# Optimization experiments

Measured on AMD Instinct MI355X. Metric: run time of the kernel, lower is better.

The kernel has to match this reference:

```python
import jax, jax.numpy as jnp
import numpy as np

B, N, C = 2, 2048, 1024
H = 16
HD = C // H  # 64


def setup_inputs() -> dict:
    key = jax.random.key(0)
    k1, k2, k3 = jax.random.split(key, 3)
    x = jax.random.normal(k1, (B, N, C), dtype=jnp.float32)
    w_qkv = jax.random.normal(k2, (C, 3 * C), dtype=jnp.float32) * (C ** -0.5)
    b_qkv = jnp.zeros((3 * C,), dtype=jnp.float32)
    w_out = jax.random.normal(k3, (C, C), dtype=jnp.float32) * (C ** -0.5)
    b_out = jnp.zeros((C,), dtype=jnp.float32)
    return {"x": x, "w_qkv": w_qkv, "b_qkv": b_qkv, "w_out": w_out, "b_out": b_out}


def reference(x, w_qkv, b_qkv, w_out, b_out):
    scale = HD ** -0.5
    # QKV projection: (B,N,3C) -> (B,N,3,H,HD) -> (B,3,H,N,HD)
    qkv = (jnp.einsum('bnc,cd->bnd', x, w_qkv) + b_qkv)
    qkv = qkv.reshape(B, N, 3, H, HD).transpose(0, 2, 3, 1, 4)
    q, k, v = qkv[:, 0], qkv[:, 1], qkv[:, 2]  # each (B,H,N,HD)
    # scaled dot-product attention with full NxN matrix (as in source)
    attn = jnp.einsum('bhnd,bhmd->bhnm', q, k) * scale
    attn = jax.nn.softmax(attn, axis=-1)
    out = jnp.einsum('bhnm,bhmd->bhnd', attn, v)  # (B,H,N,HD)
    out = out.transpose(0, 2, 1, 3).reshape(B, N, C)
    out = jnp.einsum('bnc,cd->bnd', out, w_out) + b_out
    return out
```

## Files before the change

kernel.cpp:

```cpp
#include <hip/hip_runtime.h>
#include <stdint.h>

using uint = unsigned int;
using ushort = unsigned short;

constexpr int Bb = 2;
constexpr int Ns = 2048;
constexpr int Cd = 1024;
constexpr int Hh = 16;
constexpr int HD = 64;
constexpr int BHND = Bb * Hh * Ns * HD;

constexpr float QSCL = 0.18033688f;

typedef __attribute__((ext_vector_type(8))) short short8;
typedef __attribute__((ext_vector_type(4))) float floatx4;

__device__ inline ushort f2bf(float f) {
  uint u = __float_as_uint(f);
  return (ushort)((u + 0x7fffu + ((u >> 16) & 1u)) >> 16);
}
__device__ inline ushort f2bfr(float f) {
  return (ushort)((__float_as_uint(f) + 0x8000u) >> 16);
}
__device__ inline uint cvt_pk_bf16(float lo, float hi) {
  uint r;
  asm("v_cvt_pk_bf16_f32 %0, %1, %2" : "=v"(r) : "v"(lo), "v"(hi));
  return r;
}
__device__ inline void gld_lds16(const ushort* g, ushort* l) {
  __builtin_amdgcn_global_load_lds(
      (const __attribute__((address_space(1))) uint*)g,
      (__attribute__((address_space(3))) uint*)l, 16, 0, 0);
}

__global__ __launch_bounds__(256) void prep(
    const float* __restrict__ x, ushort* __restrict__ xbf,
    const float* __restrict__ w_qkv, ushort* __restrict__ wqkvT,
    const float* __restrict__ w_out, ushort* __restrict__ woutT) {
  __shared__ alignas(16) ushort tile[32][33];
  const int bid = blockIdx.x;
  const int tid = threadIdx.x;
  if (bid < 4096) {
    const int i = bid * 256 + tid;
    const float4 v = ((const float4*)x)[i];
    ushort4 o;
    o.x = f2bf(v.x); o.y = f2bf(v.y); o.z = f2bf(v.z); o.w = f2bf(v.w);
    ((ushort4*)xbf)[i] = o;
    return;
  }
  const float* in;
  ushort* outp;
  int Cc, idx;
  if (bid < 7168) { idx = bid - 4096; in = w_qkv; outp = wqkvT; Cc = 3072; }
  else            { idx = bid - 7168; in = w_out; outp = woutT; Cc = 1024; }
  const int R = 1024;
  const int nbx = Cc >> 5;
  const int bx = idx % nbx, by = idx / nbx;
  const int c0 = bx * 32, r0 = by * 32;
  const int tx = tid & 31, ty = tid >> 5;
#pragma unroll
  for (int i = 0; i < 4; ++i)
    tile[ty + 8 * i][tx] = f2bf(in[(size_t)(r0 + ty + 8 * i) * Cc + c0 + tx]);
  __syncthreads();
#pragma unroll
  for (int i = 0; i < 4; ++i)
    outp[(size_t)(c0 + ty + 8 * i) * R + r0 + tx] = tile[tx][ty + 8 * i];
}

__global__ __launch_bounds__(256, 3) void gemm_qkv(
    const ushort* __restrict__ A, const ushort* __restrict__ Bt,
    const float* __restrict__ bias, ushort* __restrict__ outp,
    int M, int K, int Nn) {
  __shared__ alignas(16) ushort As[3][128 * 32];
  __shared__ alignas(16) ushort Bs[3][128 * 32];
  const int tid = threadIdx.x;
  const int wave = tid >> 6, lane = tid & 63;
  const int quad = lane >> 4, l16 = lane & 15;
  const int wr = wave >> 1, wc = wave & 1;
  const int m0 = blockIdx.x * 128, n0 = blockIdx.y * 128;

  const int lrow = lane >> 2;
  const int lgr = lane & 3;
  const ushort* pa = A + (size_t)(m0 + wave * 32 + lrow) * K + lgr * 8;
  const ushort* pb = Bt + (size_t)(n0 + wave * 32 + lrow) * K + lgr * 8;
  const int lofs = wave * 32 * 32;

  floatx4 acc[4][4];
#pragma unroll
  for (int i = 0; i < 4; ++i)
#pragma unroll
    for (int j = 0; j < 4; ++j) {
      acc[i][j][0] = 0.f; acc[i][j][1] = 0.f; acc[i][j][2] = 0.f; acc[i][j][3] = 0.f;
    }

  const int nkt = K >> 5;
  gld_lds16(pa, &As[0][lofs]);
  gld_lds16(pa + (size_t)16 * K, &As[0][lofs + 512]);
  gld_lds16(pb, &Bs[0][lofs]);
  gld_lds16(pb + (size_t)16 * K, &Bs[0][lofs + 512]);
  gld_lds16(pa + 32, &As[1][lofs]);
  gld_lds16(pa + 32 + (size_t)16 * K, &As[1][lofs + 512]);
  gld_lds16(pb + 32, &Bs[1][lofs]);
  gld_lds16(pb + 32 + (size_t)16 * K, &Bs[1][lofs + 512]);

  int cur = 0;
  auto compute_tile = [&](int cb) {
    short8 af[4], bfv[4];
    const ushort* Ab = &As[cb][0];
    const ushort* Bb2 = &Bs[cb][0];
#pragma unroll
    for (int mt = 0; mt < 4; ++mt)
      af[mt] = *(const short8*)&Ab[(wr * 64 + mt * 16 + l16) * 32 + quad * 8];
#pragma unroll
    for (int nt = 0; nt < 4; ++nt)
      bfv[nt] = *(const short8*)&Bb2[(wc * 64 + nt * 16 + l16) * 32 + quad * 8];
#pragma unroll
    for (int mt = 0; mt < 4; ++mt)
#pragma unroll
      for (int nt = 0; nt < 4; ++nt)
        acc[mt][nt] = __builtin_amdgcn_mfma_f32_16x16x32_bf16(af[mt], bfv[nt],
                                                              acc[mt][nt], 0, 0, 0);
  };

  for (int kt = 0; kt < nkt - 1; ++kt) {
    asm volatile("s_waitcnt vmcnt(4)" ::: "memory");
    __builtin_amdgcn_s_barrier();
    __builtin_amdgcn_sched_barrier(0);
    compute_tile(cur);
    __builtin_amdgcn_s_barrier();
    if (kt + 2 < nkt) {
      const ushort* qa = pa + (size_t)(kt + 2) * 32;
      const ushort* qb = pb + (size_t)(kt + 2) * 32;
      int nb = cur + 2; if (nb >= 3) nb -= 3;
      gld_lds16(qa, &As[nb][lofs]);
      gld_lds16(qa + (size_t)16 * K, &As[nb][lofs + 512]);
      gld_lds16(qb, &Bs[nb][lofs]);
      gld_lds16(qb + (size_t)16 * K, &Bs[nb][lofs + 512]);
    }
    ++cur; if (cur == 3) cur = 0;
  }
  asm volatile("s_waitcnt vmcnt(0)" ::: "memory");
  __builtin_amdgcn_s_barrier();
  __builtin_amdgcn_sched_barrier(0);
  compute_tile(cur);

  ushort* qp = outp;
  ushort* kp = qp + BHND;
  ushort* vp = qp + 2 * BHND;
#pragma unroll
  for (int nt = 0; nt < 4; ++nt) {
    const int gn = n0 + wc * 64 + nt * 16 + l16;
    const float bv = bias[gn];
    const int which = gn >> 10, cc = gn & 1023;
    const int h = cc >> 6, d = cc & 63;
    const float sc = (which == 0) ? QSCL : 1.0f;
#pragma unroll
    for (int mt = 0; mt < 4; ++mt) {
#pragma unroll
      for (int r = 0; r < 4; ++r) {
        const int gm = m0 + wr * 64 + mt * 16 + quad * 4 + r;
        const int b = gm >> 11, n = gm & 2047;
        const ushort o = f2bfr((acc[mt][nt][r] + bv) * sc);
        const int bh = b * Hh + h;
        if (which == 0)
          qp[((size_t)bh * Ns + n) * HD + d] = o;
        else if (which == 1)
          kp[((size_t)bh * Ns + n) * HD + d] = o;
        else
          vp[((size_t)bh * HD + d) * Ns + n] = o;
      }
    }
  }
}

__global__ __launch_bounds__(256) void gemm_out(
    const ushort* __restrict__ A, const ushort* __restrict__ Bt,
    const float* __restrict__ bias, float* __restrict__ fout,
    int M, int K, int Nn) {
  constexpr int LDT = 40;
  __shared__ alignas(16) ushort As[128 * LDT];
  __shared__ alignas(16) ushort Bs[128 * LDT];
  const int tid = threadIdx.x;
  const int wave = tid >> 6, lane = tid & 63;
  const int quad = lane >> 4, l16 = lane & 15;
  const int wr = wave >> 1, wc = wave & 1;
  const int m0 = blockIdx.x * 128, n0 = blockIdx.y * 128;

  const int srow0 = tid >> 2;
  const int skc = (tid & 3) * 8;

  const ushort* pa = A + (size_t)(m0 + srow0) * K + skc;
  const ushort* pb = Bt + (size_t)(n0 + srow0) * K + skc;

  floatx4 acc[4][4];
#pragma unroll
  for (int i = 0; i < 4; ++i)
#pragma unroll
    for (int j = 0; j < 4; ++j) {
      acc[i][j][0] = 0.f; acc[i][j][1] = 0.f; acc[i][j][2] = 0.f; acc[i][j][3] = 0.f;
    }

  uint4 ra0 = *(const uint4*)(pa);
  uint4 ra1 = *(const uint4*)(pa + (size_t)64 * K);
  uint4 rb0 = *(const uint4*)(pb);
  uint4 rb1 = *(const uint4*)(pb + (size_t)64 * K);

  const int nkt = K >> 5;
  for (int kt = 0; kt < nkt; ++kt) {
    __syncthreads();
    *(uint4*)&As[srow0 * LDT + skc] = ra0;
    *(uint4*)&As[(srow0 + 64) * LDT + skc] = ra1;
    *(uint4*)&Bs[srow0 * LDT + skc] = rb0;
    *(uint4*)&Bs[(srow0 + 64) * LDT + skc] = rb1;
    __syncthreads();
    if (kt + 1 < nkt) {
      const ushort* qa = pa + (size_t)(kt + 1) * 32;
      const ushort* qb = pb + (size_t)(kt + 1) * 32;
      ra0 = *(const uint4*)(qa);
      ra1 = *(const uint4*)(qa + (size_t)64 * K);
      rb0 = *(const uint4*)(qb);
      rb1 = *(const uint4*)(qb + (size_t)64 * K);
    }
    short8 af[4], bfv[4];
#pragma unroll
    for (int mt = 0; mt < 4; ++mt)
      af[mt] = *(const short8*)&As[(wr * 64 + mt * 16 + l16) * LDT + quad * 8];
#pragma unroll
    for (int nt = 0; nt < 4; ++nt)
      bfv[nt] = *(const short8*)&Bs[(wc * 64 + nt * 16 + l16) * LDT + quad * 8];
#pragma unroll
    for (int mt = 0; mt < 4; ++mt)
#pragma unroll
      for (int nt = 0; nt < 4; ++nt)
        acc[mt][nt] = __builtin_amdgcn_mfma_f32_16x16x32_bf16(af[mt], bfv[nt],
                                                              acc[mt][nt], 0, 0, 0);
  }

#pragma unroll
  for (int nt = 0; nt < 4; ++nt) {
    const int gn = n0 + wc * 64 + nt * 16 + l16;
    const float bv = bias[gn];
#pragma unroll
    for (int mt = 0; mt < 4; ++mt)
#pragma unroll
      for (int r = 0; r < 4; ++r) {
        const int gm = m0 + wr * 64 + mt * 16 + quad * 4 + r;
        fout[(size_t)gm * Nn + gn] = acc[mt][nt][r] + bv;
      }
  }
}

__global__ __launch_bounds__(256, 2) void attn(
    const ushort* __restrict__ q, const ushort* __restrict__ k,
    const ushort* __restrict__ vT, ushort* __restrict__ aout) {
  constexpr int LDK = 72;
  __shared__ alignas(16) ushort Ks[2][64 * LDK];
  __shared__ alignas(16) ushort Vs[2][64 * LDK];
  const int tid = threadIdx.x;
  const int wave = tid >> 6, lane = tid & 63;
  const int quad = lane >> 4, l16 = lane & 15;

  const int orig = blockIdx.x + (blockIdx.y << 4);
  const int swz = (orig & 7) * 64 + (orig >> 3);
  const int bh = swz >> 4;
  const int qw = (swz & 15) * 128 + wave * 32;

  const ushort* kb = k + (size_t)bh * Ns * HD;
  const ushort* vb = vT + (size_t)bh * HD * Ns;

  short8 aq[2][2];
#pragma unroll
  for (int nqi = 0; nqi < 2; ++nqi) {
    const ushort* qp = q + ((size_t)bh * Ns + qw + nqi * 16 + l16) * HD + quad * 8;
    aq[nqi][0] = *(const short8*)(qp);
    aq[nqi][1] = *(const short8*)(qp + 32);
  }

  floatx4 accO[4][2];
#pragma unroll
  for (int mt = 0; mt < 4; ++mt)
#pragma unroll
    for (int nqi = 0; nqi < 2; ++nqi) {
      accO[mt][nqi][0] = 0.f; accO[mt][nqi][1] = 0.f;
      accO[mt][nqi][2] = 0.f; accO[mt][nqi][3] = 0.f;
    }
  float lst[2] = {0.f, 0.f};
  const floatx4 fz = {0.f, 0.f, 0.f, 0.f};

  const int srow = tid >> 2;
  const int g0 = (tid & 3) * 2;
  const int cbA = (g0 >> 2) * 8 + ((g0 >> 1) & 1);
  const int g1 = g0 + 1;
  const int cbB = (g1 >> 2) * 8 + 4 + ((g1 >> 1) & 1);

  const ushort* kgp = kb + (size_t)srow * HD + g0 * 8;
  const ushort* vgp = vb + (size_t)srow * Ns + g0 * 8;
  const int kofs = srow * LDK + g0 * 8;
  const int vofsA = srow * LDK + cbA * 4;
  const int vofsB = srow * LDK + cbB * 4;

  uint4 kg0 = *(const uint4*)(kgp);
  uint4 kg1 = *(const uint4*)(kgp + 8);
  uint4 vg0 = *(const uint4*)(vgp);
  uint4 vg1 = *(const uint4*)(vgp + 8);
  const ushort* kpre = kgp + 64 * HD;
  const ushort* vpre = vgp + 64;

  *(uint4*)&Ks[0][kofs] = kg0;
  *(uint4*)&Ks[0][kofs + 8] = kg1;
  *(uint2*)&Vs[0][vofsA] = make_uint2(vg0.x, vg0.y);
  *(uint2*)&Vs[0][vofsA + 8] = make_uint2(vg0.z, vg0.w);
  *(uint2*)&Vs[0][vofsB] = make_uint2(vg1.x, vg1.y);
  *(uint2*)&Vs[0][vofsB + 8] = make_uint2(vg1.z, vg1.w);
  __syncthreads();

  for (int kv0 = 0; kv0 < Ns; kv0 += 128) {
#pragma unroll
    for (int half = 0; half < 2; ++half) {
      const bool more = kv0 + 64 * (half + 1) < Ns;

      short8 ak[4][2], av[4][2];
#pragma unroll
      for (int t4 = 0; t4 < 4; ++t4) {
        const int ro = (t4 * 16 + l16) * LDK + quad * 8;
        ak[t4][0] = *(const short8*)&Ks[half][ro];
        ak[t4][1] = *(const short8*)&Ks[half][ro + 32];
        av[t4][0] = *(const short8*)&Vs[half][ro];
        av[t4][1] = *(const short8*)&Vs[half][ro + 32];
      }
      if (more) {
        kg0 = *(const uint4*)(kpre);
        kg1 = *(const uint4*)(kpre + 8);
        vg0 = *(const uint4*)(vpre);
        vg1 = *(const uint4*)(vpre + 8);
        kpre += 64 * HD;
        vpre += 64;
      }

#pragma unroll
      for (int nqi = 0; nqi < 2; ++nqi) {
        floatx4 sacc[4];
        __builtin_amdgcn_s_setprio(1);
#pragma unroll
        for (int kvt = 0; kvt < 4; ++kvt)
          sacc[kvt] = __builtin_amdgcn_mfma_f32_16x16x32_bf16(
              ak[kvt][0], aq[nqi][0], fz, 0, 0, 0);
#pragma unroll
        for (int kvt = 0; kvt < 4; ++kvt)
          sacc[kvt] = __builtin_amdgcn_mfma_f32_16x16x32_bf16(
              ak[kvt][1], aq[nqi][1], sacc[kvt], 0, 0, 0);
        __builtin_amdgcn_s_setprio(0);

        uint pk[4][2];
        float ls = 0.f;
#pragma unroll
        for (int kvt = 0; kvt < 4; ++kvt) {
          const float p0 = __builtin_amdgcn_exp2f(sacc[kvt][0]);
          const float p1 = __builtin_amdgcn_exp2f(sacc[kvt][1]);
          const float p2 = __builtin_amdgcn_exp2f(sacc[kvt][2]);
          const float p3 = __builtin_amdgcn_exp2f(sacc[kvt][3]);
          ls += (p0 + p1) + (p2 + p3);
          pk[kvt][0] = cvt_pk_bf16(p0, p1);
          pk[kvt][1] = cvt_pk_bf16(p2, p3);
        }
        lst[nqi] += ls;

        __builtin_amdgcn_s_setprio(1);
#pragma unroll
        for (int ks = 0; ks < 2; ++ks) {
          union { uint u[4]; short8 s; } pf;
          pf.u[0] = pk[2 * ks][0]; pf.u[1] = pk[2 * ks][1];
          pf.u[2] = pk[2 * ks + 1][0]; pf.u[3] = pk[2 * ks + 1][1];
#pragma unroll
          for (int mt = 0; mt < 4; ++mt)
            accO[mt][nqi] = __builtin_amdgcn_mfma_f32_16x16x32_bf16(
                av[mt][ks], pf.s, accO[mt][nqi], 0, 0, 0);
        }
        __builtin_amdgcn_s_setprio(0);
      }

      if (more) {
        *(uint4*)&Ks[half ^ 1][kofs] = kg0;
        *(uint4*)&Ks[half ^ 1][kofs + 8] = kg1;
        *(uint2*)&Vs[half ^ 1][vofsA] = make_uint2(vg0.x, vg0.y);
        *(uint2*)&Vs[half ^ 1][vofsA + 8] = make_uint2(vg0.z, vg0.w);
        *(uint2*)&Vs[half ^ 1][vofsB] = make_uint2(vg1.x, vg1.y);
        *(uint2*)&Vs[half ^ 1][vofsB + 8] = make_uint2(vg1.z, vg1.w);
      }
      __syncthreads();
    }
  }

  const int b = bh >> 4, h = bh & 15;
#pragma unroll
  for (int nqi = 0; nqi < 2; ++nqi) {
    float l = lst[nqi];
    l += __shfl_xor(l, 16, 64);
    l += __shfl_xor(l, 32, 64);
    const float inv = 1.f / l;
    const int n = qw + nqi * 16 + l16;
#pragma unroll
    for (int mt = 0; mt < 4; ++mt) {
      ushort4 o;
      o.x = f2bfr(accO[mt][nqi][0] * inv);
      o.y = f2bfr(accO[mt][nqi][1] * inv);
      o.z = f2bfr(accO[mt][nqi][2] * inv);
      o.w = f2bfr(accO[mt][nqi][3] * inv);
      *(ushort4*)&aout[((size_t)(b * Ns + n)) * Cd + h * HD + mt * 16 + quad * 4] = o;
    }
  }
}

extern "C" void kernel_launch(void* const* d_in, const int* in_sizes, int n_in,
                              void* d_out, int out_size, void* d_ws, size_t ws_size,
                              hipStream_t stream) {
  (void)in_sizes; (void)n_in; (void)out_size; (void)ws_size;
  const float* x = (const float*)d_in[0];
  const float* w_qkv = (const float*)d_in[1];
  const float* b_qkv = (const float*)d_in[2];
  const float* w_out = (const float*)d_in[3];
  const float* b_out = (const float*)d_in[4];

  ushort* xbf = (ushort*)d_ws;
  ushort* wqkvT = xbf + (size_t)BHND;
  ushort* woutT = wqkvT + 3072 * 1024;
  ushort* qkvbuf = woutT + 1024 * 1024;
  ushort* aout = qkvbuf + 3 * (size_t)BHND;

  prep<<<dim3(8192), 256, 0, stream>>>(x, xbf, w_qkv, wqkvT, w_out, woutT);

  gemm_qkv<<<dim3(32, 24), 256, 0, stream>>>(xbf, wqkvT, b_qkv, qkvbuf,
                                             4096, 1024, 3072);
  attn<<<dim3(16, 32), 256, 0, stream>>>(qkvbuf, qkvbuf + BHND,
                                         qkvbuf + 2 * (size_t)BHND, aout);
  gemm_out<<<dim3(32, 8), 256, 0, stream>>>(aout, woutT, b_out, (float*)d_out,
                                            4096, 1024, 1024);
}
```

Measured before the change: 182.4 us.

## Triple-buffer output GEMM with direct global-to-LDS async loads

Restructures the output projection GEMM so each wave loads its 32-row slice of the A and B tiles straight into LDS through gld_lds16, rotating across three LDS buffers. The next tiles are prefetched two k-steps ahead, and vmcnt-based waits replace the register-staged double sync. The aim is to overlap global loads with MFMA compute, drop the VGPR staging copy, and allow two blocks per CU through launch bounds. The padded LDS stride is removed, which may bring bank conflicts back on the fragment reads.

```diff
diff --git a/kernel.cpp b/kernel.cpp
--- a/kernel.cpp
+++ b/kernel.cpp
@@ -174,24 +174,23 @@
   }
 }
 
-__global__ __launch_bounds__(256) void gemm_out(
+__global__ __launch_bounds__(256, 2) void gemm_out(
     const ushort* __restrict__ A, const ushort* __restrict__ Bt,
     const float* __restrict__ bias, float* __restrict__ fout,
     int M, int K, int Nn) {
-  constexpr int LDT = 40;
-  __shared__ alignas(16) ushort As[128 * LDT];
-  __shared__ alignas(16) ushort Bs[128 * LDT];
+  __shared__ alignas(16) ushort As[3][128 * 32];
+  __shared__ alignas(16) ushort Bs[3][128 * 32];
   const int tid = threadIdx.x;
   const int wave = tid >> 6, lane = tid & 63;
   const int quad = lane >> 4, l16 = lane & 15;
   const int wr = wave >> 1, wc = wave & 1;
   const int m0 = blockIdx.x * 128, n0 = blockIdx.y * 128;
 
-  const int srow0 = tid >> 2;
-  const int skc = (tid & 3) * 8;
-
-  const ushort* pa = A + (size_t)(m0 + srow0) * K + skc;
-  const ushort* pb = Bt + (size_t)(n0 + srow0) * K + skc;
+  const int lrow = lane >> 2;
+  const int lgr = lane & 3;
+  const ushort* pa = A + (size_t)(m0 + wave * 32 + lrow) * K + lgr * 8;
+  const ushort* pb = Bt + (size_t)(n0 + wave * 32 + lrow) * K + lgr * 8;
+  const int lofs = wave * 32 * 32;
 
   floatx4 acc[4][4];
 #pragma unroll
@@ -201,41 +200,56 @@
       acc[i][j][0] = 0.f; acc[i][j][1] = 0.f; acc[i][j][2] = 0.f; acc[i][j][3] = 0.f;
     }
 
-  uint4 ra0 = *(const uint4*)(pa);
-  uint4 ra1 = *(const uint4*)(pa + (size_t)64 * K);
-  uint4 rb0 = *(const uint4*)(pb);
-  uint4 rb1 = *(const uint4*)(pb + (size_t)64 * K);
-
   const int nkt = K >> 5;
-  for (int kt = 0; kt < nkt; ++kt) {
-    __syncthreads();
-    *(uint4*)&As[srow0 * LDT + skc] = ra0;
-    *(uint4*)&As[(srow0 + 64) * LDT + skc] = ra1;
-    *(uint4*)&Bs[srow0 * LDT + skc] = rb0;
-    *(uint4*)&Bs[(srow0 + 64) * LDT + skc] = rb1;
-    __syncthreads();
-    if (kt + 1 < nkt) {
-      const ushort* qa = pa + (size_t)(kt + 1) * 32;
-      const ushort* qb = pb + (size_t)(kt + 1) * 32;
-      ra0 = *(const uint4*)(qa);
-      ra1 = *(const uint4*)(qa + (size_t)64 * K);
-      rb0 = *(const uint4*)(qb);
-      rb1 = *(const uint4*)(qb + (size_t)64 * K);
-    }
+  gld_lds16(pa, &As[0][lofs]);
+  gld_lds16(pa + (size_t)16 * K, &As[0][lofs + 512]);
+  gld_lds16(pb, &Bs[0][lofs]);
+  gld_lds16(pb + (size_t)16 * K, &Bs[0][lofs + 512]);
+  gld_lds16(pa + 32, &As[1][lofs]);
+  gld_lds16(pa + 32 + (size_t)16 * K, &As[1][lofs + 512]);
+  gld_lds16(pb + 32, &Bs[1][lofs]);
+  gld_lds16(pb + 32 + (size_t)16 * K, &Bs[1][lofs + 512]);
+
+  int cur = 0;
+  auto compute_tile = [&](int cb) {
     short8 af[4], bfv[4];
+    const ushort* Ab = &As[cb][0];
+    const ushort* Bb2 = &Bs[cb][0];
 #pragma unroll
     for (int mt = 0; mt < 4; ++mt)
-      af[mt] = *(const short8*)&As[(wr * 64 + mt * 16 + l16) * LDT + quad * 8];
+      af[mt] = *(const short8*)&Ab[(wr * 64 + mt * 16 + l16) * 32 + quad * 8];
 #pragma unroll
     for (int nt = 0; nt < 4; ++nt)
-      bfv[nt] = *(const short8*)&Bs[(wc * 64 + nt * 16 + l16) * LDT + quad * 8];
+      bfv[nt] = *(const short8*)&Bb2[(wc * 64 + nt * 16 + l16) * 32 + quad * 8];
 #pragma unroll
     for (int mt = 0; mt < 4; ++mt)
 #pragma unroll
       for (int nt = 0; nt < 4; ++nt)
         acc[mt][nt] = __builtin_amdgcn_mfma_f32_16x16x32_bf16(af[mt], bfv[nt],
                                                               acc[mt][nt], 0, 0, 0);
-  }
+  };
+
+  for (int kt = 0; kt < nkt - 1; ++kt) {
+    asm volatile("s_waitcnt vmcnt(4)" ::: "memory");
+    __builtin_amdgcn_s_barrier();
+    __builtin_amdgcn_sched_barrier(0);
+    compute_tile(cur);
+    __builtin_amdgcn_s_barrier();
+    if (kt + 2 < nkt) {
+      const ushort* qa = pa + (size_t)(kt + 2) * 32;
+      const ushort* qb = pb + (size_t)(kt + 2) * 32;
+      int nb = cur + 2; if (nb >= 3) nb -= 3;
+      gld_lds16(qa, &As[nb][lofs]);
+      gld_lds16(qa + (size_t)16 * K, &As[nb][lofs + 512]);
+      gld_lds16(qb, &Bs[nb][lofs]);
+      gld_lds16(qb + (size_t)16 * K, &Bs[nb][lofs + 512]);
+    }
+    ++cur; if (cur == 3) cur = 0;
+  }
+  asm volatile("s_waitcnt vmcnt(0)" ::: "memory");
+  __builtin_amdgcn_s_barrier();
+  __builtin_amdgcn_sched_barrier(0);
+  compute_tile(cur);
 
 #pragma unroll
   for (int nt = 0; nt < 4; ++nt) {
```

Measured after the change: 181.8 us. Within noise of the previous version (-0.3%).
